# Performance work log

Hardware: AMD Instinct MI355X
Metric: run time of the kernel (lower is better)

Reference implementation:

```python
import jax, jax.numpy as jnp
import numpy as np

B, T, F, H = 2048, 512, 32, 128  # batch, seq_len, input_features, hidden_units

def _xavier(key, shape):
    fan_in, fan_out = shape[1], shape[0]
    limit = float(np.sqrt(6.0 / (fan_in + fan_out)))
    return jax.random.uniform(key, shape, jnp.float32, -limit, limit)

def setup_inputs() -> dict:
    key = jax.random.key(0)
    ks = jax.random.split(key, 8)
    x = jax.random.normal(ks[0], (B, T, F), jnp.float32)
    # PyTorch LSTM weights: weight_ih_l{k} [4H, in], weight_hh_l{k} [4H, H]; biases init to zeros.
    Wih0 = _xavier(ks[1], (4 * H, F))
    Whh0 = _xavier(ks[2], (4 * H, H))
    b0 = jnp.zeros((4 * H,), jnp.float32)  # b_ih + b_hh (both zero-init)
    Wih1 = _xavier(ks[3], (4 * H, H))
    Whh1 = _xavier(ks[4], (4 * H, H))
    b1 = jnp.zeros((4 * H,), jnp.float32)
    Wfc = _xavier(ks[5], (1, H))
    bfc = jnp.zeros((1,), jnp.float32)
    return dict(x=x, Wih0=Wih0, Whh0=Whh0, b0=b0, Wih1=Wih1, Whh1=Whh1, b1=b1, Wfc=Wfc, bfc=bfc)

def _lstm_layer(x, Wih, Whh, b):
    # x: [B, T, Din] -> outputs h over time: [B, T, H]
    pre = jnp.einsum('btf,gf->btg', x, Wih) + b  # precompute input projections [B, T, 4H]
    h0 = jnp.zeros((x.shape[0], Whh.shape[1]), x.dtype)

    def step(carry, p_t):
        h, c = carry
        z = p_t + h @ Whh.T  # [B, 4H]
        i, f, g, o = jnp.split(z, 4, axis=-1)  # PyTorch gate order: i, f, g, o
        i = jax.nn.sigmoid(i)
        f = jax.nn.sigmoid(f)
        g = jnp.tanh(g)
        o = jax.nn.sigmoid(o)
        c = f * c + i * g
        h = o * jnp.tanh(c)
        return (h, c), h

    (_, _), hs = jax.lax.scan(step, (h0, h0), jnp.swapaxes(pre, 0, 1))  # hs: [T, B, H]
    return jnp.swapaxes(hs, 0, 1)

def reference(x, Wih0, Whh0, b0, Wih1, Whh1, b1, Wfc, bfc):
    h = _lstm_layer(x, Wih0, Whh0, b0)   # layer 0 (dropout off in eval)
    h = _lstm_layer(h, Wih1, Whh1, b1)   # layer 1
    last = h[:, -1, :]                   # [B, H]
    return last @ Wfc.T + bfc            # [B, 1]
```

## Files before the change

kernel.cpp:

```cpp
#include <hip/hip_runtime.h>
#include <stdint.h>


#define B_ 2048
#define T_ 512
#define F_ 32
#define H_ 128
#define LSTR 144
#define H0SZ (8 * LSTR)
#define W1SLOT 512
#define W1WAVE (32 * W1SLOT)

#define LOG2E 1.4426950408889634f

typedef _Float16 half8 __attribute__((ext_vector_type(8)));
typedef float float4_t __attribute__((ext_vector_type(4)));

#define BARRIER_LGKM() asm volatile("s_waitcnt lgkmcnt(0)\n\ts_barrier" ::: "memory")

__device__ __forceinline__ float fexp2(float x) {
  float r; asm("v_exp_f32 %0, %1" : "=v"(r) : "v"(x)); return r;
}
__device__ __forceinline__ float frcp(float x) { return __builtin_amdgcn_rcpf(x); }

__device__ __forceinline__ half8 cvt2f4(float4_t a, float4_t b) {
  half8 r;
  r[0] = (_Float16)a[0]; r[1] = (_Float16)a[1]; r[2] = (_Float16)a[2]; r[3] = (_Float16)a[3];
  r[4] = (_Float16)b[0]; r[5] = (_Float16)b[1]; r[6] = (_Float16)b[2]; r[7] = (_Float16)b[3];
  return r;
}
__device__ __forceinline__ half8 load8cvt(const float* p) {
  return cvt2f4(*(const float4_t*)p, *(const float4_t*)(p + 4));
}

__global__ __launch_bounds__(512, 2) void lstm_fused(
    const float* __restrict__ x, const float* __restrict__ Wih0,
    const float* __restrict__ Whh0, const float* __restrict__ b0,
    const float* __restrict__ Wih1, const float* __restrict__ Whh1,
    const float* __restrict__ b1, const float* __restrict__ Wfc,
    const float* __restrict__ bfc, float* __restrict__ out)
{
  __shared__ __attribute__((aligned(16))) _Float16 lds_w1[4 * W1WAVE];
  __shared__ __attribute__((aligned(16))) _Float16 lds_h0[2 * H0SZ];
  __shared__ __attribute__((aligned(16))) _Float16 lds_h1[2 * H0SZ];
  __shared__ float lds_fc[8][8];

  const int tid  = threadIdx.x;
  const int w    = tid >> 6;
  const int lane = tid & 63;
  const int n    = lane & 15;
  const int q    = lane >> 4;
  const int rbase = (int)blockIdx.x * 8;
  const int rsh  = (q >> 1) * 2;
  const int rowq = (q & 1) * 4;
  const int wq   = w >> 1;
  const int hc0  = wq * 16 + n;
  const int hc1  = hc0 + 64;
  const int aoff = (n & 7) * LSTR + q * 8;
  const bool isL0 = ((w & 1) == 0);

  for (int i = tid; i < 2 * H0SZ; i += 512) lds_h1[i] = (_Float16)0.0f;

  const float4_t zC = {0.f, 0.f, 0.f, 0.f};

  auto GATES = [&](const float4_t (&acc)[4], float cI, float cF, float cG,
                   float cO, float& ca, float& cb, _Float16* dst, int hcol) {
#pragma unroll
    for (int rr = 0; rr < 2; ++rr) {
      const int ri = rsh + rr;
      const float gi = frcp(1.0f + fexp2(__builtin_fmaf(acc[0][ri], -LOG2E, cI)));
      const float gf = frcp(1.0f + fexp2(__builtin_fmaf(acc[1][ri], -LOG2E, cF)));
      const float gg = 1.0f - 2.0f * frcp(1.0f + fexp2(__builtin_fmaf(acc[2][ri], 2.0f * LOG2E, cG)));
      const float go = frcp(1.0f + fexp2(__builtin_fmaf(acc[3][ri], -LOG2E, cO)));
      float& cc = rr ? cb : ca;
      cc = __builtin_fmaf(gf, cc, gi * gg);
      const float th = 1.0f - 2.0f * frcp(1.0f + fexp2(cc * (2.0f * LOG2E)));
      dst[(rowq + ri) * LSTR + hcol] = (_Float16)(go * th);
    }
  };

  if (isL0) {
    half8 bwih0[2][4], bwhh0[2][4][4];
    float cI[2], cF[2], cG[2], cO[2];
#pragma unroll
    for (int grp = 0; grp < 2; ++grp) {
      const int hcol = grp ? hc1 : hc0;
#pragma unroll
      for (int gt = 0; gt < 4; ++gt) {
        const int g = gt * H_ + hcol;
        bwih0[grp][gt] = load8cvt(Wih0 + g * F_ + q * 8);
#pragma unroll
        for (int kc = 0; kc < 4; ++kc)
          bwhh0[grp][gt][kc] = load8cvt(Whh0 + g * H_ + kc * 32 + q * 8);
      }
      cI[grp] = -b0[0 * H_ + hcol] * LOG2E;
      cF[grp] = -b0[1 * H_ + hcol] * LOG2E;
      cG[grp] =  b0[2 * H_ + hcol] * (2.0f * LOG2E);
      cO[grp] = -b0[3 * H_ + hcol] * LOG2E;
    }
    float c0a[2] = {0.f, 0.f}, c0b[2] = {0.f, 0.f};

    const float* xptr = x + (rbase + (n & 7)) * (T_ * F_) + q * 8;
    float4_t xrA = *(const float4_t*)(xptr);
    float4_t xrB = *(const float4_t*)(xptr + 4);

    {
      half8 ax = cvt2f4(xrA, xrB);
#pragma unroll
      for (int grp = 0; grp < 2; ++grp) {
        float4_t acc[4];
#pragma unroll
        for (int gt = 0; gt < 4; ++gt)
          acc[gt] = __builtin_amdgcn_mfma_f32_16x16x32_f16(ax, bwih0[grp][gt], zC, 0, 0, 0);
        GATES(acc, cI[grp], cF[grp], cG[grp], cO[grp], c0a[grp], c0b[grp],
              lds_h0 , grp ? hc1 : hc0);
      }
      xrA = *(const float4_t*)(xptr + F_);
      xrB = *(const float4_t*)(xptr + F_ + 4);
      BARRIER_LGKM();
    }

#pragma unroll 1
    for (int tau = 1; tau < T_; ++tau) {
      const int pw = tau & 1;
      _Float16* h0rd = lds_h0 + (pw ^ 1) * H0SZ;
      _Float16* h0wr = lds_h0 + pw * H0SZ;

      half8 ah[4];
#pragma unroll
      for (int kc = 0; kc < 4; ++kc)
        ah[kc] = *(const half8*)(h0rd + aoff + kc * 32);
      half8 ax = cvt2f4(xrA, xrB);

#pragma unroll
      for (int grp = 0; grp < 2; ++grp) {
        float4_t acc[4];
#pragma unroll
        for (int gt = 0; gt < 4; ++gt)
          acc[gt] = __builtin_amdgcn_mfma_f32_16x16x32_f16(ax, bwih0[grp][gt], zC, 0, 0, 0);
#pragma unroll
        for (int kc = 0; kc < 4; ++kc)
#pragma unroll
          for (int gt = 0; gt < 4; ++gt)
            acc[gt] = __builtin_amdgcn_mfma_f32_16x16x32_f16(ah[kc], bwhh0[grp][gt][kc], acc[gt], 0, 0, 0);
        if (grp == 0) {
          const int tn = (tau + 1 < T_) ? tau + 1 : T_ - 1;
          xrA = *(const float4_t*)(xptr + tn * F_);
          xrB = *(const float4_t*)(xptr + tn * F_ + 4);
        }
        GATES(acc, cI[grp], cF[grp], cG[grp], cO[grp], c0a[grp], c0b[grp],
              h0wr, grp ? hc1 : hc0);
      }
      BARRIER_LGKM();
    }
  } else {
    half8 bwhh1[2][4][4];
    float cI[2], cF[2], cG[2], cO[2];
    _Float16* w1base = lds_w1 + wq * W1WAVE + q * 128 + n * 8;
#pragma unroll
    for (int grp = 0; grp < 2; ++grp) {
      const int hcol = grp ? hc1 : hc0;
#pragma unroll
      for (int gt = 0; gt < 4; ++gt) {
        const int g = gt * H_ + hcol;
#pragma unroll
        for (int kc = 0; kc < 4; ++kc) {
          bwhh1[grp][gt][kc] = load8cvt(Whh1 + g * H_ + kc * 32 + q * 8);
          *(half8*)(w1base + (grp * 16 + kc * 4 + gt) * W1SLOT) =
              load8cvt(Wih1 + g * H_ + kc * 32 + q * 8);
        }
      }
      cI[grp] = -b1[0 * H_ + hcol] * LOG2E;
      cF[grp] = -b1[1 * H_ + hcol] * LOG2E;
      cG[grp] =  b1[2 * H_ + hcol] * (2.0f * LOG2E);
      cO[grp] = -b1[3 * H_ + hcol] * LOG2E;
    }
    float c1a[2] = {0.f, 0.f}, c1b[2] = {0.f, 0.f};

    BARRIER_LGKM();

#pragma unroll 1
    for (int tau = 1; tau < T_; ++tau) {
      const int pw = tau & 1;
      _Float16* h0rd = lds_h0 + (pw ^ 1) * H0SZ;
      _Float16* h1rd = lds_h1 + pw * H0SZ;
      _Float16* h1wr = lds_h1 + (pw ^ 1) * H0SZ;

      half8 ah[4], a1h[4];
#pragma unroll
      for (int kc = 0; kc < 4; ++kc) {
        ah[kc]  = *(const half8*)(h0rd + aoff + kc * 32);
        a1h[kc] = *(const half8*)(h1rd + aoff + kc * 32);
      }
#pragma unroll
      for (int grp = 0; grp < 2; ++grp) {
        half8 wa[4], wb[4];
        float4_t acc[4];
#pragma unroll
        for (int gt = 0; gt < 4; ++gt)
          wa[gt] = *(const half8*)(w1base + (grp * 16 + 0 * 4 + gt) * W1SLOT);
#pragma unroll
        for (int gt = 0; gt < 4; ++gt)
          wb[gt] = *(const half8*)(w1base + (grp * 16 + 1 * 4 + gt) * W1SLOT);
#pragma unroll
        for (int gt = 0; gt < 4; ++gt)
          acc[gt] = __builtin_amdgcn_mfma_f32_16x16x32_f16(ah[0], wa[gt], zC, 0, 0, 0);
#pragma unroll
        for (int gt = 0; gt < 4; ++gt)
          wa[gt] = *(const half8*)(w1base + (grp * 16 + 2 * 4 + gt) * W1SLOT);
#pragma unroll
        for (int gt = 0; gt < 4; ++gt)
          acc[gt] = __builtin_amdgcn_mfma_f32_16x16x32_f16(ah[1], wb[gt], acc[gt], 0, 0, 0);
#pragma unroll
        for (int gt = 0; gt < 4; ++gt)
          wb[gt] = *(const half8*)(w1base + (grp * 16 + 3 * 4 + gt) * W1SLOT);
#pragma unroll
        for (int gt = 0; gt < 4; ++gt)
          acc[gt] = __builtin_amdgcn_mfma_f32_16x16x32_f16(ah[2], wa[gt], acc[gt], 0, 0, 0);
#pragma unroll
        for (int gt = 0; gt < 4; ++gt)
          acc[gt] = __builtin_amdgcn_mfma_f32_16x16x32_f16(ah[3], wb[gt], acc[gt], 0, 0, 0);
#pragma unroll
        for (int kc = 0; kc < 4; ++kc)
#pragma unroll
          for (int gt = 0; gt < 4; ++gt)
            acc[gt] = __builtin_amdgcn_mfma_f32_16x16x32_f16(a1h[kc], bwhh1[grp][gt][kc], acc[gt], 0, 0, 0);
        GATES(acc, cI[grp], cF[grp], cG[grp], cO[grp], c1a[grp], c1b[grp],
              h1wr, grp ? hc1 : hc0);
      }
      BARRIER_LGKM();
    }

    {
      _Float16* h0rd = lds_h0 + H0SZ;
      _Float16* h1rd = lds_h1;
      _Float16* h1wr = lds_h1 + H0SZ;

      half8 ah[4], a1h[4];
#pragma unroll
      for (int kc = 0; kc < 4; ++kc) {
        ah[kc]  = *(const half8*)(h0rd + aoff + kc * 32);
        a1h[kc] = *(const half8*)(h1rd + aoff + kc * 32);
      }
#pragma unroll
      for (int grp = 0; grp < 2; ++grp) {
        half8 wa[4], wb[4];
        float4_t acc[4];
#pragma unroll
        for (int gt = 0; gt < 4; ++gt)
          wa[gt] = *(const half8*)(w1base + (grp * 16 + 0 * 4 + gt) * W1SLOT);
#pragma unroll
        for (int gt = 0; gt < 4; ++gt)
          wb[gt] = *(const half8*)(w1base + (grp * 16 + 1 * 4 + gt) * W1SLOT);
#pragma unroll
        for (int gt = 0; gt < 4; ++gt)
          acc[gt] = __builtin_amdgcn_mfma_f32_16x16x32_f16(ah[0], wa[gt], zC, 0, 0, 0);
#pragma unroll
        for (int gt = 0; gt < 4; ++gt)
          wa[gt] = *(const half8*)(w1base + (grp * 16 + 2 * 4 + gt) * W1SLOT);
#pragma unroll
        for (int gt = 0; gt < 4; ++gt)
          acc[gt] = __builtin_amdgcn_mfma_f32_16x16x32_f16(ah[1], wb[gt], acc[gt], 0, 0, 0);
#pragma unroll
        for (int gt = 0; gt < 4; ++gt)
          wb[gt] = *(const half8*)(w1base + (grp * 16 + 3 * 4 + gt) * W1SLOT);
#pragma unroll
        for (int gt = 0; gt < 4; ++gt)
          acc[gt] = __builtin_amdgcn_mfma_f32_16x16x32_f16(ah[2], wa[gt], acc[gt], 0, 0, 0);
#pragma unroll
        for (int gt = 0; gt < 4; ++gt)
          acc[gt] = __builtin_amdgcn_mfma_f32_16x16x32_f16(ah[3], wb[gt], acc[gt], 0, 0, 0);
#pragma unroll
        for (int kc = 0; kc < 4; ++kc)
#pragma unroll
          for (int gt = 0; gt < 4; ++gt)
            acc[gt] = __builtin_amdgcn_mfma_f32_16x16x32_f16(a1h[kc], bwhh1[grp][gt][kc], acc[gt], 0, 0, 0);
        GATES(acc, cI[grp], cF[grp], cG[grp], cO[grp], c1a[grp], c1b[grp],
              h1wr, grp ? hc1 : hc0);
      }
      asm volatile("s_waitcnt lgkmcnt(0)" ::: "memory");
    }
  }

  __syncthreads();

  const int colg = w * 16 + n;
  const float wfcv = Wfc[colg];
  float p0 = (float)lds_h1[H0SZ + q * LSTR + colg] * wfcv;
  float p1 = (float)lds_h1[H0SZ + (q + 4) * LSTR + colg] * wfcv;
#pragma unroll
  for (int m = 1; m < 16; m <<= 1) {
    p0 += __shfl_xor(p0, m);
    p1 += __shfl_xor(p1, m);
  }
  if (n == 0) {
    lds_fc[w][q] = p0;
    lds_fc[w][q + 4] = p1;
  }
  __syncthreads();
  if (tid < 8) {
    float s = bfc[0];
#pragma unroll
    for (int wv = 0; wv < 8; ++wv) s += lds_fc[wv][tid];
    out[rbase + tid] = s;
  }
}

extern "C" void kernel_launch(void* const* d_in, const int* in_sizes, int n_in,
                              void* d_out, int out_size, void* d_ws, size_t ws_size,
                              hipStream_t stream) {
  const float* x    = (const float*)d_in[0];
  const float* Wih0 = (const float*)d_in[1];
  const float* Whh0 = (const float*)d_in[2];
  const float* b0   = (const float*)d_in[3];
  const float* Wih1 = (const float*)d_in[4];
  const float* Whh1 = (const float*)d_in[5];
  const float* b1   = (const float*)d_in[6];
  const float* Wfc  = (const float*)d_in[7];
  const float* bfc  = (const float*)d_in[8];
  float* outp = (float*)d_out;
  (void)d_ws; (void)ws_size;

  lstm_fused<<<B_ / 8, 512, 0, stream>>>(x, Wih0, Whh0, b0, Wih1, Whh1, b1,
                                         Wfc, bfc, outp);
}
```

Baseline: 1.041 ms.

## Merge layer-0 and layer-1 work into each wave with 256-thread blocks

Instead of splitting waves into dedicated layer-0 and layer-1 roles across 512 threads, each of 4 waves now computes both layers sequentially per timestep, halving the block size. More weights are held in registers, with part of Wih1 and Wih0 staged in LDS, and the bias constants are packed as fp16. The intent is to cut per-step barrier participants and idle imbalance between layer roles. In exchange each wave's serial critical path per step roughly doubles, register pressure rises, and fp16 biases lose precision.

```diff
diff --git a/kernel.cpp b/kernel.cpp
--- a/kernel.cpp
+++ b/kernel.cpp
@@ -8,8 +8,8 @@
 #define H_ 128
 #define LSTR 144
 #define H0SZ (8 * LSTR)
-#define W1SLOT 512
-#define W1WAVE (32 * W1SLOT)
+#define W0WAVE 4096
+#define W1WAVE 8192
 
 #define LOG2E 1.4426950408889634f
 
@@ -33,17 +33,18 @@
   return cvt2f4(*(const float4_t*)p, *(const float4_t*)(p + 4));
 }
 
-__global__ __launch_bounds__(512, 2) void lstm_fused(
+__global__ __launch_bounds__(256, 1) void lstm_fused(
     const float* __restrict__ x, const float* __restrict__ Wih0,
     const float* __restrict__ Whh0, const float* __restrict__ b0,
     const float* __restrict__ Wih1, const float* __restrict__ Whh1,
     const float* __restrict__ b1, const float* __restrict__ Wfc,
     const float* __restrict__ bfc, float* __restrict__ out)
 {
+  __shared__ __attribute__((aligned(16))) _Float16 lds_w0[4 * W0WAVE];
   __shared__ __attribute__((aligned(16))) _Float16 lds_w1[4 * W1WAVE];
   __shared__ __attribute__((aligned(16))) _Float16 lds_h0[2 * H0SZ];
   __shared__ __attribute__((aligned(16))) _Float16 lds_h1[2 * H0SZ];
-  __shared__ float lds_fc[8][8];
+  __shared__ float lds_fc[4][8];
 
   const int tid  = threadIdx.x;
   const int w    = tid >> 6;
@@ -53,18 +54,58 @@
   const int rbase = (int)blockIdx.x * 8;
   const int rsh  = (q >> 1) * 2;
   const int rowq = (q & 1) * 4;
-  const int wq   = w >> 1;
-  const int hc0  = wq * 16 + n;
+  const int hc0  = w * 16 + n;
   const int hc1  = hc0 + 64;
   const int aoff = (n & 7) * LSTR + q * 8;
-  const bool isL0 = ((w & 1) == 0);
-
-  for (int i = tid; i < 2 * H0SZ; i += 512) lds_h1[i] = (_Float16)0.0f;
+
+  half8 bwhh0[2][4][4], bwhh1[2][4][4], bwih1r[2][2][4];
+  _Float16* w0base = lds_w0 + w * W0WAVE + q * 128 + n * 8;
+  _Float16* w1base = lds_w1 + w * W1WAVE + q * 128 + n * 8;
+  half8 cpk0, cpk1;
+#pragma unroll
+  for (int grp = 0; grp < 2; ++grp) {
+    const int hcol = grp ? hc1 : hc0;
+#pragma unroll
+    for (int gt = 0; gt < 4; ++gt) {
+      const int g = gt * H_ + hcol;
+      *(half8*)(w0base + (grp * 4 + gt) * 512) = load8cvt(Wih0 + g * F_ + q * 8);
+#pragma unroll
+      for (int kc = 0; kc < 4; ++kc) {
+        bwhh0[grp][gt][kc] = load8cvt(Whh0 + g * H_ + kc * 32 + q * 8);
+        bwhh1[grp][gt][kc] = load8cvt(Whh1 + g * H_ + kc * 32 + q * 8);
+      }
+      bwih1r[grp][0][gt] = load8cvt(Wih1 + g * H_ + 0 * 32 + q * 8);
+      bwih1r[grp][1][gt] = load8cvt(Wih1 + g * H_ + 1 * 32 + q * 8);
+      *(half8*)(w1base + (grp * 8 + gt) * 512)     = load8cvt(Wih1 + g * H_ + 2 * 32 + q * 8);
+      *(half8*)(w1base + (grp * 8 + 4 + gt) * 512) = load8cvt(Wih1 + g * H_ + 3 * 32 + q * 8);
+    }
+    cpk0[grp * 4 + 0] = (_Float16)(-b0[0 * H_ + hcol] * LOG2E);
+    cpk0[grp * 4 + 1] = (_Float16)(-b0[1 * H_ + hcol] * LOG2E);
+    cpk0[grp * 4 + 2] = (_Float16)( b0[2 * H_ + hcol] * (2.0f * LOG2E));
+    cpk0[grp * 4 + 3] = (_Float16)(-b0[3 * H_ + hcol] * LOG2E);
+    cpk1[grp * 4 + 0] = (_Float16)(-b1[0 * H_ + hcol] * LOG2E);
+    cpk1[grp * 4 + 1] = (_Float16)(-b1[1 * H_ + hcol] * LOG2E);
+    cpk1[grp * 4 + 2] = (_Float16)( b1[2 * H_ + hcol] * (2.0f * LOG2E));
+    cpk1[grp * 4 + 3] = (_Float16)(-b1[3 * H_ + hcol] * LOG2E);
+  }
+
+  for (int i = tid; i < 2 * H0SZ; i += 256) lds_h1[i] = (_Float16)0.0f;
+  __syncthreads();
 
   const float4_t zC = {0.f, 0.f, 0.f, 0.f};
-
-  auto GATES = [&](const float4_t (&acc)[4], float cI, float cF, float cG,
-                   float cO, float& ca, float& cb, _Float16* dst, int hcol) {
+  float c0a[2] = {0.f, 0.f}, c0b[2] = {0.f, 0.f};
+  float c1a[2] = {0.f, 0.f}, c1b[2] = {0.f, 0.f};
+
+  const float* xptr = x + (rbase + (n & 7)) * (T_ * F_) + q * 8;
+  float4_t xrA = *(const float4_t*)(xptr);
+  float4_t xrB = *(const float4_t*)(xptr + 4);
+
+  auto GATES = [&](const float4_t (&acc)[4], half8 cpk, int grp, float& ca,
+                   float& cb, _Float16* dst, int hcol) {
+    const float cI = (float)cpk[grp * 4 + 0];
+    const float cF = (float)cpk[grp * 4 + 1];
+    const float cG = (float)cpk[grp * 4 + 2];
+    const float cO = (float)cpk[grp * 4 + 3];
 #pragma unroll
     for (int rr = 0; rr < 2; ++rr) {
       const int ri = rsh + rr;
@@ -79,215 +120,127 @@
     }
   };
 
-  if (isL0) {
-    half8 bwih0[2][4], bwhh0[2][4][4];
-    float cI[2], cF[2], cG[2], cO[2];
+  auto L1STEP = [&](const half8 (&ah)[4], _Float16* h1rd, _Float16* h1wr) {
+    half8 a1h[4];
+#pragma unroll
+    for (int kc = 0; kc < 4; ++kc)
+      a1h[kc] = *(const half8*)(h1rd + aoff + kc * 32);
 #pragma unroll
     for (int grp = 0; grp < 2; ++grp) {
-      const int hcol = grp ? hc1 : hc0;
-#pragma unroll
-      for (int gt = 0; gt < 4; ++gt) {
-        const int g = gt * H_ + hcol;
-        bwih0[grp][gt] = load8cvt(Wih0 + g * F_ + q * 8);
-#pragma unroll
-        for (int kc = 0; kc < 4; ++kc)
-          bwhh0[grp][gt][kc] = load8cvt(Whh0 + g * H_ + kc * 32 + q * 8);
+      half8 wA[4], wB[4];
+      float4_t acc[4];
+#pragma unroll
+      for (int gt = 0; gt < 4; ++gt)
+        wA[gt] = *(const half8*)(w1base + (grp * 8 + gt) * 512);
+#pragma unroll
+      for (int gt = 0; gt < 4; ++gt)
+        acc[gt] = __builtin_amdgcn_mfma_f32_16x16x32_f16(ah[0], bwih1r[grp][0][gt], zC, 0, 0, 0);
+#pragma unroll
+      for (int gt = 0; gt < 4; ++gt)
+        acc[gt] = __builtin_amdgcn_mfma_f32_16x16x32_f16(ah[1], bwih1r[grp][1][gt], acc[gt], 0, 0, 0);
+#pragma unroll
+      for (int gt = 0; gt < 4; ++gt)
+        wB[gt] = *(const half8*)(w1base + (grp * 8 + 4 + gt) * 512);
+#pragma unroll
+      for (int gt = 0; gt < 4; ++gt)
+        acc[gt] = __builtin_amdgcn_mfma_f32_16x16x32_f16(ah[2], wA[gt], acc[gt], 0, 0, 0);
+#pragma unroll
+      for (int gt = 0; gt < 4; ++gt)
+        acc[gt] = __builtin_amdgcn_mfma_f32_16x16x32_f16(ah[3], wB[gt], acc[gt], 0, 0, 0);
+#pragma unroll
+      for (int kc = 0; kc < 4; ++kc)
+#pragma unroll
+        for (int gt = 0; gt < 4; ++gt)
+          acc[gt] = __builtin_amdgcn_mfma_f32_16x16x32_f16(a1h[kc], bwhh1[grp][gt][kc], acc[gt], 0, 0, 0);
+      GATES(acc, cpk1, grp, c1a[grp], c1b[grp], h1wr, grp ? hc1 : hc0);
+    }
+  };
+
+  {
+    half8 w0w[4];
+#pragma unroll
+    for (int gt = 0; gt < 4; ++gt)
+      w0w[gt] = *(const half8*)(w0base + gt * 512);
+    half8 ax = cvt2f4(xrA, xrB);
+#pragma unroll
+    for (int grp = 0; grp < 2; ++grp) {
+      float4_t acc[4];
+#pragma unroll
+      for (int gt = 0; gt < 4; ++gt)
+        acc[gt] = __builtin_amdgcn_mfma_f32_16x16x32_f16(ax, w0w[gt], zC, 0, 0, 0);
+      if (grp == 0) {
+#pragma unroll
+        for (int gt = 0; gt < 4; ++gt)
+          w0w[gt] = *(const half8*)(w0base + (4 + gt) * 512);
       }
-      cI[grp] = -b0[0 * H_ + hcol] * LOG2E;
-      cF[grp] = -b0[1 * H_ + hcol] * LOG2E;
-      cG[grp] =  b0[2 * H_ + hcol] * (2.0f * LOG2E);
-      cO[grp] = -b0[3 * H_ + hcol] * LOG2E;
-    }
-    float c0a[2] = {0.f, 0.f}, c0b[2] = {0.f, 0.f};
-
-    const float* xptr = x + (rbase + (n & 7)) * (T_ * F_) + q * 8;
-    float4_t xrA = *(const float4_t*)(xptr);
-    float4_t xrB = *(const float4_t*)(xptr + 4);
-
-    {
-      half8 ax = cvt2f4(xrA, xrB);
-#pragma unroll
-      for (int grp = 0; grp < 2; ++grp) {
-        float4_t acc[4];
-#pragma unroll
-        for (int gt = 0; gt < 4; ++gt)
-          acc[gt] = __builtin_amdgcn_mfma_f32_16x16x32_f16(ax, bwih0[grp][gt], zC, 0, 0, 0);
-        GATES(acc, cI[grp], cF[grp], cG[grp], cO[grp], c0a[grp], c0b[grp],
-              lds_h0 , grp ? hc1 : hc0);
+      GATES(acc, cpk0, grp, c0a[grp], c0b[grp], lds_h0 , grp ? hc1 : hc0);
+    }
+    xrA = *(const float4_t*)(xptr + F_);
+    xrB = *(const float4_t*)(xptr + F_ + 4);
+    BARRIER_LGKM();
+  }
+
+#pragma unroll 1
+  for (int tau = 1; tau < T_; ++tau) {
+    const int pw = tau & 1;
+    _Float16* h0rd = lds_h0 + (pw ^ 1) * H0SZ;
+    _Float16* h0wr = lds_h0 + pw * H0SZ;
+    _Float16* h1rd = lds_h1 + pw * H0SZ;
+    _Float16* h1wr = lds_h1 + (pw ^ 1) * H0SZ;
+
+    half8 ah[4];
+#pragma unroll
+    for (int kc = 0; kc < 4; ++kc)
+      ah[kc] = *(const half8*)(h0rd + aoff + kc * 32);
+    half8 w0w[4];
+#pragma unroll
+    for (int gt = 0; gt < 4; ++gt)
+      w0w[gt] = *(const half8*)(w0base + gt * 512);
+    half8 ax = cvt2f4(xrA, xrB);
+
+#pragma unroll
+    for (int grp = 0; grp < 2; ++grp) {
+      float4_t acc[4];
+#pragma unroll
+      for (int gt = 0; gt < 4; ++gt)
+        acc[gt] = __builtin_amdgcn_mfma_f32_16x16x32_f16(ax, w0w[gt], zC, 0, 0, 0);
+#pragma unroll
+      for (int kc = 0; kc < 4; ++kc)
+#pragma unroll
+        for (int gt = 0; gt < 4; ++gt)
+          acc[gt] = __builtin_amdgcn_mfma_f32_16x16x32_f16(ah[kc], bwhh0[grp][gt][kc], acc[gt], 0, 0, 0);
+      if (grp == 0) {
+#pragma unroll
+        for (int gt = 0; gt < 4; ++gt)
+          w0w[gt] = *(const half8*)(w0base + (4 + gt) * 512);
+        const int tn = (tau + 1 < T_) ? tau + 1 : T_ - 1;
+        xrA = *(const float4_t*)(xptr + tn * F_);
+        xrB = *(const float4_t*)(xptr + tn * F_ + 4);
       }
-      xrA = *(const float4_t*)(xptr + F_);
-      xrB = *(const float4_t*)(xptr + F_ + 4);
-      BARRIER_LGKM();
-    }
-
-#pragma unroll 1
-    for (int tau = 1; tau < T_; ++tau) {
-      const int pw = tau & 1;
-      _Float16* h0rd = lds_h0 + (pw ^ 1) * H0SZ;
-      _Float16* h0wr = lds_h0 + pw * H0SZ;
-
-      half8 ah[4];
-#pragma unroll
-      for (int kc = 0; kc < 4; ++kc)
-        ah[kc] = *(const half8*)(h0rd + aoff + kc * 32);
-      half8 ax = cvt2f4(xrA, xrB);
-
-#pragma unroll
-      for (int grp = 0; grp < 2; ++grp) {
-        float4_t acc[4];
-#pragma unroll
-        for (int gt = 0; gt < 4; ++gt)
-          acc[gt] = __builtin_amdgcn_mfma_f32_16x16x32_f16(ax, bwih0[grp][gt], zC, 0, 0, 0);
-#pragma unroll
-        for (int kc = 0; kc < 4; ++kc)
-#pragma unroll
-          for (int gt = 0; gt < 4; ++gt)
-            acc[gt] = __builtin_amdgcn_mfma_f32_16x16x32_f16(ah[kc], bwhh0[grp][gt][kc], acc[gt], 0, 0, 0);
-        if (grp == 0) {
-          const int tn = (tau + 1 < T_) ? tau + 1 : T_ - 1;
-          xrA = *(const float4_t*)(xptr + tn * F_);
-          xrB = *(const float4_t*)(xptr + tn * F_ + 4);
-        }
-        GATES(acc, cI[grp], cF[grp], cG[grp], cO[grp], c0a[grp], c0b[grp],
-              h0wr, grp ? hc1 : hc0);
-      }
-      BARRIER_LGKM();
-    }
-  } else {
-    half8 bwhh1[2][4][4];
-    float cI[2], cF[2], cG[2], cO[2];
-    _Float16* w1base = lds_w1 + wq * W1WAVE + q * 128 + n * 8;
-#pragma unroll
-    for (int grp = 0; grp < 2; ++grp) {
-      const int hcol = grp ? hc1 : hc0;
-#pragma unroll
-      for (int gt = 0; gt < 4; ++gt) {
-        const int g = gt * H_ + hcol;
-#pragma unroll
-        for (int kc = 0; kc < 4; ++kc) {
-          bwhh1[grp][gt][kc] = load8cvt(Whh1 + g * H_ + kc * 32 + q * 8);
-          *(half8*)(w1base + (grp * 16 + kc * 4 + gt) * W1SLOT) =
-              load8cvt(Wih1 + g * H_ + kc * 32 + q * 8);
-        }
-      }
-      cI[grp] = -b1[0 * H_ + hcol] * LOG2E;
-      cF[grp] = -b1[1 * H_ + hcol] * LOG2E;
-      cG[grp] =  b1[2 * H_ + hcol] * (2.0f * LOG2E);
-      cO[grp] = -b1[3 * H_ + hcol] * LOG2E;
-    }
-    float c1a[2] = {0.f, 0.f}, c1b[2] = {0.f, 0.f};
-
+      GATES(acc, cpk0, grp, c0a[grp], c0b[grp], h0wr, grp ? hc1 : hc0);
+    }
+
+    L1STEP(ah, h1rd, h1wr);
     BARRIER_LGKM();
-
-#pragma unroll 1
-    for (int tau = 1; tau < T_; ++tau) {
-      const int pw = tau & 1;
-      _Float16* h0rd = lds_h0 + (pw ^ 1) * H0SZ;
-      _Float16* h1rd = lds_h1 + pw * H0SZ;
-      _Float16* h1wr = lds_h1 + (pw ^ 1) * H0SZ;
-
-      half8 ah[4], a1h[4];
-#pragma unroll
-      for (int kc = 0; kc < 4; ++kc) {
-        ah[kc]  = *(const half8*)(h0rd + aoff + kc * 32);
-        a1h[kc] = *(const half8*)(h1rd + aoff + kc * 32);
-      }
-#pragma unroll
-      for (int grp = 0; grp < 2; ++grp) {
-        half8 wa[4], wb[4];
-        float4_t acc[4];
-#pragma unroll
-        for (int gt = 0; gt < 4; ++gt)
-          wa[gt] = *(const half8*)(w1base + (grp * 16 + 0 * 4 + gt) * W1SLOT);
-#pragma unroll
-        for (int gt = 0; gt < 4; ++gt)
-          wb[gt] = *(const half8*)(w1base + (grp * 16 + 1 * 4 + gt) * W1SLOT);
-#pragma unroll
-        for (int gt = 0; gt < 4; ++gt)
-          acc[gt] = __builtin_amdgcn_mfma_f32_16x16x32_f16(ah[0], wa[gt], zC, 0, 0, 0);
-#pragma unroll
-        for (int gt = 0; gt < 4; ++gt)
-          wa[gt] = *(const half8*)(w1base + (grp * 16 + 2 * 4 + gt) * W1SLOT);
-#pragma unroll
-        for (int gt = 0; gt < 4; ++gt)
-          acc[gt] = __builtin_amdgcn_mfma_f32_16x16x32_f16(ah[1], wb[gt], acc[gt], 0, 0, 0);
-#pragma unroll
-        for (int gt = 0; gt < 4; ++gt)
-          wb[gt] = *(const half8*)(w1base + (grp * 16 + 3 * 4 + gt) * W1SLOT);
-#pragma unroll
-        for (int gt = 0; gt < 4; ++gt)
-          acc[gt] = __builtin_amdgcn_mfma_f32_16x16x32_f16(ah[2], wa[gt], acc[gt], 0, 0, 0);
-#pragma unroll
-        for (int gt = 0; gt < 4; ++gt)
-          acc[gt] = __builtin_amdgcn_mfma_f32_16x16x32_f16(ah[3], wb[gt], acc[gt], 0, 0, 0);
-#pragma unroll
-        for (int kc = 0; kc < 4; ++kc)
-#pragma unroll
-          for (int gt = 0; gt < 4; ++gt)
-            acc[gt] = __builtin_amdgcn_mfma_f32_16x16x32_f16(a1h[kc], bwhh1[grp][gt][kc], acc[gt], 0, 0, 0);
-        GATES(acc, cI[grp], cF[grp], cG[grp], cO[grp], c1a[grp], c1b[grp],
-              h1wr, grp ? hc1 : hc0);
-      }
-      BARRIER_LGKM();
-    }
-
-    {
-      _Float16* h0rd = lds_h0 + H0SZ;
-      _Float16* h1rd = lds_h1;
-      _Float16* h1wr = lds_h1 + H0SZ;
-
-      half8 ah[4], a1h[4];
-#pragma unroll
-      for (int kc = 0; kc < 4; ++kc) {
-        ah[kc]  = *(const half8*)(h0rd + aoff + kc * 32);
-        a1h[kc] = *(const half8*)(h1rd + aoff + kc * 32);
-      }
-#pragma unroll
-      for (int grp = 0; grp < 2; ++grp) {
-        half8 wa[4], wb[4];
-        float4_t acc[4];
-#pragma unroll
-        for (int gt = 0; gt < 4; ++gt)
-          wa[gt] = *(const half8*)(w1base + (grp * 16 + 0 * 4 + gt) * W1SLOT);
-#pragma unroll
-        for (int gt = 0; gt < 4; ++gt)
-          wb[gt] = *(const half8*)(w1base + (grp * 16 + 1 * 4 + gt) * W1SLOT);
-#pragma unroll
-        for (int gt = 0; gt < 4; ++gt)
-          acc[gt] = __builtin_amdgcn_mfma_f32_16x16x32_f16(ah[0], wa[gt], zC, 0, 0, 0);
-#pragma unroll
-        for (int gt = 0; gt < 4; ++gt)
-          wa[gt] = *(const half8*)(w1base + (grp * 16 + 2 * 4 + gt) * W1SLOT);
-#pragma unroll
-        for (int gt = 0; gt < 4; ++gt)
-          acc[gt] = __builtin_amdgcn_mfma_f32_16x16x32_f16(ah[1], wb[gt], acc[gt], 0, 0, 0);
-#pragma unroll
-        for (int gt = 0; gt < 4; ++gt)
-          wb[gt] = *(const half8*)(w1base + (grp * 16 + 3 * 4 + gt) * W1SLOT);
-#pragma unroll
-        for (int gt = 0; gt < 4; ++gt)
-          acc[gt] = __builtin_amdgcn_mfma_f32_16x16x32_f16(ah[2], wa[gt], acc[gt], 0, 0, 0);
-#pragma unroll
-        for (int gt = 0; gt < 4; ++gt)
-          acc[gt] = __builtin_amdgcn_mfma_f32_16x16x32_f16(ah[3], wb[gt], acc[gt], 0, 0, 0);
-#pragma unroll
-        for (int kc = 0; kc < 4; ++kc)
-#pragma unroll
-          for (int gt = 0; gt < 4; ++gt)
-            acc[gt] = __builtin_amdgcn_mfma_f32_16x16x32_f16(a1h[kc], bwhh1[grp][gt][kc], acc[gt], 0, 0, 0);
-        GATES(acc, cI[grp], cF[grp], cG[grp], cO[grp], c1a[grp], c1b[grp],
-              h1wr, grp ? hc1 : hc0);
-      }
-      asm volatile("s_waitcnt lgkmcnt(0)" ::: "memory");
-    }
-  }
-
+  }
+
+  {
+    _Float16* h0rd = lds_h0 + H0SZ;
+    _Float16* h1rd = lds_h1;
+    _Float16* h1wr = lds_h1 + H0SZ;
+    half8 ah[4];
+#pragma unroll
+    for (int kc = 0; kc < 4; ++kc)
+      ah[kc] = *(const half8*)(h0rd + aoff + kc * 32);
+    L1STEP(ah, h1rd, h1wr);
+  }
   __syncthreads();
 
-  const int colg = w * 16 + n;
-  const float wfcv = Wfc[colg];
-  float p0 = (float)lds_h1[H0SZ + q * LSTR + colg] * wfcv;
-  float p1 = (float)lds_h1[H0SZ + (q + 4) * LSTR + colg] * wfcv;
+  const float wf0 = Wfc[hc0], wf1 = Wfc[hc1];
+  float p0 = (float)lds_h1[H0SZ + q * LSTR + hc0] * wf0
+           + (float)lds_h1[H0SZ + q * LSTR + hc1] * wf1;
+  float p1 = (float)lds_h1[H0SZ + (q + 4) * LSTR + hc0] * wf0
+           + (float)lds_h1[H0SZ + (q + 4) * LSTR + hc1] * wf1;
 #pragma unroll
   for (int m = 1; m < 16; m <<= 1) {
     p0 += __shfl_xor(p0, m);
@@ -301,7 +254,7 @@
   if (tid < 8) {
     float s = bfc[0];
 #pragma unroll
-    for (int wv = 0; wv < 8; ++wv) s += lds_fc[wv][tid];
+    for (int wv = 0; wv < 4; ++wv) s += lds_fc[wv][tid];
     out[rbase + tid] = s;
   }
 }
@@ -321,6 +274,6 @@
   float* outp = (float*)d_out;
   (void)d_ws; (void)ws_size;
 
-  lstm_fused<<<B_ / 8, 512, 0, stream>>>(x, Wih0, Whh0, b0, Wih1, Whh1, b1,
+  lstm_fused<<<B_ / 8, 256, 0, stream>>>(x, Wih0, Whh0, b0, Wih1, Whh1, b1,
                                          Wfc, bfc, outp);
 }
```

Measured after the change: 1.637 ms. 57.3% more time.
